# Kernel tuning notes

Hardware: AMD Instinct MI355X
Metric: run time of the kernel (lower is better)

## Reference

```python
import jax, jax.numpy as jnp
import numpy as np

STATE_DIM, FAST, SLOW, ACT, HID = 256, 32, 16, 4, 256
B, T = 256, 512


def _gelu(x):
    return jax.nn.gelu(x, approximate=False)


def _gru_cell(x, h, wih, whh, bih, bhh):
    # torch GRUCell: r,z,n gates; weights are [3H, in]/[3H, H]
    gi = x @ wih.T + bih
    gh = h @ whh.T + bhh
    ir, iz, inn = jnp.split(gi, 3, axis=-1)
    hr, hz, hn = jnp.split(gh, 3, axis=-1)
    r = jax.nn.sigmoid(ir + hr)
    z = jax.nn.sigmoid(iz + hz)
    n = jnp.tanh(inn + r * hn)
    return (1.0 - z) * n + z * h


def setup_inputs() -> dict:
    key = jax.random.key(0)
    ks = jax.random.split(key, 32)
    s = 0.05
    d = {
        'states': jax.random.normal(ks[0], (B, T, STATE_DIM), jnp.float32),
        'actions': jax.random.normal(ks[1], (B, T, ACT), jnp.float32),
        'noise_fast': jax.random.normal(ks[2], (B, T, FAST), jnp.float32),
        'noise_slow': jax.random.normal(ks[3], (B, T, SLOW), jnp.float32),
        # fast encoder: Linear(256,256) GELU Linear(256,64)
        'fe_w1': jax.random.normal(ks[4], (HID, STATE_DIM)) * s,
        'fe_b1': jnp.zeros((HID,)),
        'fe_w2': jax.random.normal(ks[5], (FAST * 2, HID)) * s,
        'fe_b2': jnp.zeros((FAST * 2,)),
        # fast GRUCell(in=36, h=32)
        'fg_wih': jax.random.normal(ks[6], (3 * FAST, FAST + ACT)) * s,
        'fg_whh': jax.random.normal(ks[7], (3 * FAST, FAST)) * s,
        'fg_bih': jnp.zeros((3 * FAST,)),
        'fg_bhh': jnp.zeros((3 * FAST,)),
        # slow encoder: Linear(288,128) GELU Linear(128,32)
        'se_w1': jax.random.normal(ks[8], (HID // 2, STATE_DIM + FAST)) * s,
        'se_b1': jnp.zeros((HID // 2,)),
        'se_w2': jax.random.normal(ks[9], (SLOW * 2, HID // 2)) * s,
        'se_b2': jnp.zeros((SLOW * 2,)),
        # slow GRUCell(in=48, h=16)
        'sg_wih': jax.random.normal(ks[10], (3 * SLOW, SLOW + FAST)) * s,
        'sg_whh': jax.random.normal(ks[11], (3 * SLOW, SLOW)) * s,
        'sg_bih': jnp.zeros((3 * SLOW,)),
        'sg_bhh': jnp.zeros((3 * SLOW,)),
        # decoder: Linear(48,256) GELU Linear(256,256)
        'de_w1': jax.random.normal(ks[12], (HID, FAST + SLOW)) * s,
        'de_b1': jnp.zeros((HID,)),
        'de_w2': jax.random.normal(ks[13], (STATE_DIM, HID)) * s,
        'de_b2': jnp.zeros((STATE_DIM,)),
        'slow_update_rate': jnp.asarray(0.1, jnp.float32),
    }
    return d


def _forward(states, actions, noise_fast, noise_slow,
             fe_w1, fe_b1, fe_w2, fe_b2, fg_wih, fg_whh, fg_bih, fg_bhh,
             se_w1, se_b1, se_w2, se_b2, sg_wih, sg_whh, sg_bih, sg_bhh,
             de_w1, de_b1, de_w2, de_b2, slow_update_rate):
    Bn = states.shape[0]
    upd = jax.nn.sigmoid(slow_update_rate)

    def step(carry, xs):
        z_fast, z_slow = carry
        state, action, nf, ns = xs  # [B, ...] per-timestep slices
        # fast encoder + reparameterization
        fp = _gelu(state @ fe_w1.T + fe_b1) @ fe_w2.T + fe_b2
        f_mean, f_lv = jnp.split(fp, 2, axis=-1)
        z_fast_new = f_mean + jnp.exp(0.5 * f_lv) * nf
        z_fast = _gru_cell(jnp.concatenate([z_fast_new, action], -1), z_fast,
                           fg_wih, fg_whh, fg_bih, fg_bhh)
        # slow encoder + reparameterization
        sp = _gelu(jnp.concatenate([state, z_fast], -1) @ se_w1.T + se_b1) @ se_w2.T + se_b2
        s_mean, s_lv = jnp.split(sp, 2, axis=-1)
        z_slow_new = s_mean + jnp.exp(0.5 * s_lv) * ns
        z_slow_trans = _gru_cell(jnp.concatenate([z_slow_new, z_fast], -1), z_slow,
                                 sg_wih, sg_whh, sg_bih, sg_bhh)
        z_slow = upd * z_slow_trans + (1.0 - upd) * z_slow
        # decoder
        pred = _gelu(jnp.concatenate([z_fast, z_slow], -1) @ de_w1.T + de_b1) @ de_w2.T + de_b2
        return (z_fast, z_slow), (z_fast, z_slow, pred)

    init = (jnp.zeros((Bn, FAST), states.dtype), jnp.zeros((Bn, SLOW), states.dtype))
    xs = (states.swapaxes(0, 1), actions.swapaxes(0, 1),
          noise_fast.swapaxes(0, 1), noise_slow.swapaxes(0, 1))  # time-major [T,B,*]
    _, (zf, zs, preds) = jax.lax.scan(step, init, xs)
    return (preds.swapaxes(0, 1), zf.swapaxes(0, 1), zs.swapaxes(0, 1))


def reference(states, actions, noise_fast, noise_slow,
              fe_w1, fe_b1, fe_w2, fe_b2, fg_wih, fg_whh, fg_bih, fg_bhh,
              se_w1, se_b1, se_w2, se_b2, sg_wih, sg_whh, sg_bih, sg_bhh,
              de_w1, de_b1, de_w2, de_b2, slow_update_rate):
    # returns (predictions [B,T,state_dim], fast_latents [B,T,32], slow_latents [B,T,16])
    return _forward(states, actions, noise_fast, noise_slow,
                    fe_w1, fe_b1, fe_w2, fe_b2, fg_wih, fg_whh, fg_bih, fg_bhh,
                    se_w1, se_b1, se_w2, se_b2, sg_wih, sg_whh, sg_bih, sg_bhh,
                    de_w1, de_b1, de_w2, de_b2, slow_update_rate)
```

## Files before the change

kernel.cpp:

```cpp
#include <hip/hip_runtime.h>

typedef unsigned short u16t;
typedef __attribute__((ext_vector_type(8))) short bf16x8;
typedef __attribute__((ext_vector_type(4))) float f32x4;

#define DI static __device__ __forceinline__

constexpr int Bn = 256, Tn = 512;
constexpr long Rn = (long)Bn * Tn;

DI float b2f(u16t u){ union{unsigned u32; float f;} v; v.u32 = ((unsigned)u)<<16; return v.f; }
DI u16t f2b(float f){ union{float fp; unsigned u;} v; v.fp=f; return (u16t)((v.u + 0x7fffu + ((v.u>>16)&1u))>>16); }
DI float fsigm(float x){ return __builtin_amdgcn_rcpf(1.f + __expf(-x)); }
DI float ftanh(float x){ float e = __expf(2.f*x); return 1.f - 2.f*__builtin_amdgcn_rcpf(e+1.f); }
DI float fgelu(float x){
  float t = 0.7978845608028654f*x*(1.f + 0.044715f*x*x);
  return x*(1.f - __builtin_amdgcn_rcpf(__expf(2.f*t)+1.f));
}
DI f32x4 mfma16(bf16x8 a, bf16x8 b, f32x4 c){ return __builtin_amdgcn_mfma_f32_16x16x32_bf16(a,b,c,0,0,0); }
DI bf16x8 ldw8(const float* p){
  f32x4 a = *(const f32x4*)p, b = *(const f32x4*)(p+4);
  bf16x8 o;
  o[0]=(short)f2b(a[0]); o[1]=(short)f2b(a[1]); o[2]=(short)f2b(a[2]); o[3]=(short)f2b(a[3]);
  o[4]=(short)f2b(b[0]); o[5]=(short)f2b(b[1]); o[6]=(short)f2b(b[2]); o[7]=(short)f2b(b[3]);
  return o;
}
DI bf16x8 zero8(){ bf16x8 v; v[0]=0;v[1]=0;v[2]=0;v[3]=0;v[4]=0;v[5]=0;v[6]=0;v[7]=0; return v; }

__global__ __launch_bounds__(256) void k_pre(
    const float* __restrict__ states, const float* __restrict__ nfast,
    const float* __restrict__ fe_w1, const float* __restrict__ fe_b1,
    const float* __restrict__ fe_w2, const float* __restrict__ fe_b2,
    const float* __restrict__ se_w1, const float* __restrict__ se_b1,
    u16t* __restrict__ ws_zfn, u16t* __restrict__ ws_se1)
{
  __shared__ __align__(16) u16t s_x[64*256];
  __shared__ __align__(16) u16t s_h[64*256];
  const int tid = threadIdx.x;
  const int lane = tid & 63, wave = tid >> 6;
  const int l15 = lane & 15, lh = lane >> 4;
  const long row0 = (long)blockIdx.x * 64;

  #pragma unroll
  for (int i=0;i<8;i++){
    int c = tid + i*256;
    int row = c >> 5, col = (c & 31) << 3;
    bf16x8 v = ldw8(states + (row0+row)*256 + col);
    *(bf16x8*)&s_x[row*256 + (col ^ ((row&7)<<3))] = v;
  }
  __syncthreads();

  const int wrow = wave*16;
  const int arow = wrow + l15;
  f32x4 acc1[16], acc3[8];
  #pragma unroll
  for (int nt=0;nt<16;nt++){ float bv = fe_b1[nt*16+l15]; acc1[nt] = (f32x4){bv,bv,bv,bv}; }
  #pragma unroll
  for (int nt=0;nt<8;nt++){ float bv = se_b1[nt*16+l15]; acc3[nt] = (f32x4){bv,bv,bv,bv}; }
  #pragma unroll
  for (int kt=0;kt<8;kt++){
    int acol = kt*32 + lh*8;
    bf16x8 af = *(const bf16x8*)&s_x[arow*256 + (acol ^ ((arow&7)<<3))];
    #pragma unroll
    for (int nt=0;nt<16;nt++){
      bf16x8 bw = ldw8(fe_w1 + (nt*16+l15)*256 + acol);
      acc1[nt] = mfma16(af, bw, acc1[nt]);
    }
    #pragma unroll
    for (int nt=0;nt<8;nt++){
      bf16x8 bw = ldw8(se_w1 + (nt*16+l15)*288 + acol);
      acc3[nt] = mfma16(af, bw, acc3[nt]);
    }
  }
  #pragma unroll
  for (int nt=0;nt<8;nt++){
    #pragma unroll
    for (int r=0;r<4;r++){
      int row = wrow + lh*4 + r;
      ws_se1[(row0+row)*128 + nt*16+l15] = f2b(acc3[nt][r]);
    }
  }
  #pragma unroll
  for (int nt=0;nt<16;nt++){
    #pragma unroll
    for (int r=0;r<4;r++){
      int row = wrow + lh*4 + r; int col = nt*16 + l15;
      s_h[row*256 + (col ^ ((row&7)<<3))] = f2b(fgelu(acc1[nt][r]));
    }
  }
  __syncthreads();
  f32x4 acc2[4];
  #pragma unroll
  for (int a=0;a<4;a++){ float bv = fe_b2[a*16+l15]; acc2[a] = (f32x4){bv,bv,bv,bv}; }
  #pragma unroll
  for (int kt=0;kt<8;kt++){
    int acol = kt*32 + lh*8;
    bf16x8 af = *(const bf16x8*)&s_h[arow*256 + (acol ^ ((arow&7)<<3))];
    #pragma unroll
    for (int a=0;a<4;a++){
      bf16x8 bw = ldw8(fe_w2 + (a*16+l15)*256 + acol);
      acc2[a] = mfma16(af, bw, acc2[a]);
    }
  }
  #pragma unroll
  for (int a=0;a<2;a++){
    #pragma unroll
    for (int r=0;r<4;r++){
      int row = wrow + lh*4 + r; int col = a*16 + l15;
      float nfv = nfast[(row0+row)*32 + col];
      float zv = acc2[a][r] + __expf(0.5f*acc2[a+2][r])*nfv;
      ws_zfn[(row0+row)*32 + col] = f2b(zv);
    }
  }
}

__global__ __launch_bounds__(64,1) void k_rec(
  const u16t* __restrict__ ws_zfn, const u16t* __restrict__ ws_se1,
  const float* __restrict__ actions, const float* __restrict__ noise_slow,
  const float* __restrict__ fg_wih, const float* __restrict__ fg_whh,
  const float* __restrict__ fg_bih, const float* __restrict__ fg_bhh,
  const float* __restrict__ se_w1, const float* __restrict__ se_w2, const float* __restrict__ se_b2,
  const float* __restrict__ sg_wih, const float* __restrict__ sg_whh,
  const float* __restrict__ sg_bih, const float* __restrict__ sg_bhh,
  const float* __restrict__ updp,
  float* __restrict__ out_zf, float* __restrict__ out_zs)
{
  __shared__ __align__(16) u16t  zfa [16*64];
  __shared__ __align__(16) u16t  hzf [16*64];
  __shared__ __align__(16) u16t  se1b[16*128];
  __shared__ __align__(16) float nsb [16*16];
  __shared__ __align__(16) u16t  hidb[16*128];
  __shared__ __align__(16) u16t  zsb2[16*32];
  const int lane = threadIdx.x;
  const int l15 = lane & 15, lh = lane >> 4;
  const long b0 = (long)blockIdx.x * 16;

  bf16x8 Fwih[6][2], Fwhh[6], Fsw1[8], Fsw2[2][4], Fsgi[3][2], Fsgh[3];
  #pragma unroll
  for (int nt=0;nt<6;nt++){
    Fwih[nt][0] = ldw8(fg_wih + (nt*16+l15)*36 + lh*8);
    bf16x8 v = zero8();
    if (lh==0){
      #pragma unroll
      for (int e=0;e<4;e++) v[e] = (short)f2b(fg_wih[(nt*16+l15)*36 + 32 + e]);
    }
    Fwih[nt][1] = v;
    Fwhh[nt] = ldw8(fg_whh + (nt*16+l15)*32 + lh*8);
  }
  #pragma unroll
  for (int nt=0;nt<8;nt++) Fsw1[nt] = ldw8(se_w1 + (nt*16+l15)*288 + 256 + lh*8);
  #pragma unroll
  for (int nt=0;nt<2;nt++){
    #pragma unroll
    for (int kt=0;kt<4;kt++) Fsw2[nt][kt] = ldw8(se_w2 + (nt*16+l15)*128 + kt*32 + lh*8);
  }
  #pragma unroll
  for (int nt=0;nt<3;nt++){
    #pragma unroll
    for (int kt=0;kt<2;kt++){
      bf16x8 v = zero8();
      if (!(kt==1 && lh>=2)) v = ldw8(sg_wih + (nt*16+l15)*48 + kt*32 + lh*8);
      Fsgi[nt][kt] = v;
    }
    {
      bf16x8 v = zero8();
      if (lh < 2) v = ldw8(sg_whh + (nt*16+l15)*16 + lh*8);
      Fsgh[nt] = v;
    }
  }
  float bih_c[6], bhh_c[6], seb2_c[2], sgbi_c[3], sgbh_c[3];
  #pragma unroll
  for (int nt=0;nt<6;nt++){ bih_c[nt] = fg_bih[nt*16+l15]; bhh_c[nt] = fg_bhh[nt*16+l15]; }
  #pragma unroll
  for (int nt=0;nt<2;nt++) seb2_c[nt] = se_b2[nt*16+l15];
  #pragma unroll
  for (int nt=0;nt<3;nt++){ sgbi_c[nt]=sg_bih[nt*16+l15]; sgbh_c[nt]=sg_bhh[nt*16+l15]; }
  const float upd = fsigm(updp[0]);

  for (int e=0;e<16;e++){ zfa[lane*16+e]=0; hzf[lane*16+e]=0; }
  for (int e=0;e<8;e++) zsb2[lane*8+e]=0;
  float zf_r[2][4] = {{0,0,0,0},{0,0,0,0}};
  float zs_r[4] = {0,0,0,0};

  bf16x8 pf_zfn, pf_se[4]; float pf_act; f32x4 pf_ns;
  const int prow = lane >> 2, pq = lane & 3;
  auto pfload = [&](int tt){
    pf_zfn = *(const bf16x8*)(ws_zfn + ((b0+prow)*Tn + tt)*32 + pq*8);
    #pragma unroll
    for (int i=0;i<4;i++){ int c = i*64+lane; int row = c>>4; int off=(c&15)*8;
      pf_se[i] = *(const bf16x8*)(ws_se1 + ((b0+row)*Tn + tt)*128 + off); }
    pf_act = actions[((b0+prow)*Tn + tt)*4 + pq];
    pf_ns  = *(const f32x4*)(noise_slow + ((b0+prow)*Tn + tt)*16 + pq*4);
  };
  pfload(0);

  for (int t=0; t<Tn; t++){
    *(bf16x8*)&zfa[prow*64 + pq*8] = pf_zfn;
    zfa[prow*64 + 32 + pq] = f2b(pf_act);
    #pragma unroll
    for (int i=0;i<4;i++) *(bf16x8*)&se1b[(i*64+lane)*8] = pf_se[i];
    *(f32x4*)&nsb[prow*16 + pq*4] = pf_ns;
    __syncthreads();
    if (t+1 < Tn) pfload(t+1);

    {
      f32x4 gi[6], gh[6];
      #pragma unroll
      for (int nt=0;nt<6;nt++){ float bi=bih_c[nt], bh=bhh_c[nt];
        gi[nt]=(f32x4){bi,bi,bi,bi}; gh[nt]=(f32x4){bh,bh,bh,bh}; }
      #pragma unroll
      for (int kt=0;kt<2;kt++){
        bf16x8 ax = *(const bf16x8*)&zfa[l15*64 + kt*32 + lh*8];
        #pragma unroll
        for (int nt=0;nt<6;nt++) gi[nt] = mfma16(ax, Fwih[nt][kt], gi[nt]);
      }
      {
        bf16x8 az = *(const bf16x8*)&hzf[l15*64 + 16 + lh*8];
        #pragma unroll
        for (int nt=0;nt<6;nt++) gh[nt] = mfma16(az, Fwhh[nt], gh[nt]);
      }
      #pragma unroll
      for (int a=0;a<2;a++){
        #pragma unroll
        for (int r=0;r<4;r++){
          int row = lh*4+r; int cg = a*16+l15;
          float rg = fsigm(gi[a][r]   + gh[a][r]);
          float zg = fsigm(gi[2+a][r] + gh[2+a][r]);
          float ng = ftanh(gi[4+a][r] + rg*gh[4+a][r]);
          float hv = (1.f-zg)*ng + zg*zf_r[a][r];
          zf_r[a][r] = hv;
          hzf[row*64 + 16 + cg] = f2b(hv);
          out_zf[((b0+row)*Tn + t)*32 + cg] = hv;
        }
      }
    }
    __syncthreads();
    {
      bf16x8 azf2 = *(const bf16x8*)&hzf[l15*64 + 16 + lh*8];
      f32x4 se[8];
      #pragma unroll
      for (int nt=0;nt<8;nt++){
        f32x4 c;
        #pragma unroll
        for (int r=0;r<4;r++) c[r] = b2f(se1b[(lh*4+r)*128 + nt*16+l15]);
        se[nt] = mfma16(azf2, Fsw1[nt], c);
      }
      #pragma unroll
      for (int nt=0;nt<8;nt++){
        #pragma unroll
        for (int r=0;r<4;r++)
          hidb[(lh*4+r)*128 + nt*16+l15] = f2b(fgelu(se[nt][r]));
      }
    }
    __syncthreads();
    {
      f32x4 sp[2];
      #pragma unroll
      for (int nt=0;nt<2;nt++){ float bv=seb2_c[nt]; sp[nt]=(f32x4){bv,bv,bv,bv}; }
      #pragma unroll
      for (int kt=0;kt<4;kt++){
        bf16x8 ah = *(const bf16x8*)&hidb[l15*128 + kt*32 + lh*8];
        #pragma unroll
        for (int nt=0;nt<2;nt++) sp[nt] = mfma16(ah, Fsw2[nt][kt], sp[nt]);
      }
      #pragma unroll
      for (int r=0;r<4;r++){
        int row = lh*4+r;
        float nsv = nsb[row*16 + l15];
        float zn = sp[0][r] + __expf(0.5f*sp[1][r])*nsv;
        hzf[row*64 + l15] = f2b(zn);
      }
    }
    __syncthreads();
    {
      f32x4 gi2[3], gh2[3];
      #pragma unroll
      for (int nt=0;nt<3;nt++){ float bi=sgbi_c[nt], bh=sgbh_c[nt];
        gi2[nt]=(f32x4){bi,bi,bi,bi}; gh2[nt]=(f32x4){bh,bh,bh,bh}; }
      {
        bf16x8 azs = *(const bf16x8*)&zsb2[l15*32 + lh*8];
        #pragma unroll
        for (int nt=0;nt<3;nt++) gh2[nt] = mfma16(azs, Fsgh[nt], gh2[nt]);
      }
      #pragma unroll
      for (int kt=0;kt<2;kt++){
        bf16x8 ax = *(const bf16x8*)&hzf[l15*64 + kt*32 + lh*8];
        #pragma unroll
        for (int nt=0;nt<3;nt++) gi2[nt] = mfma16(ax, Fsgi[nt][kt], gi2[nt]);
      }
      #pragma unroll
      for (int r=0;r<4;r++){
        int row = lh*4+r;
        float rg = fsigm(gi2[0][r] + gh2[0][r]);
        float zg = fsigm(gi2[1][r] + gh2[1][r]);
        float ng = ftanh(gi2[2][r] + rg*gh2[2][r]);
        float zt = (1.f-zg)*ng + zg*zs_r[r];
        float zn = upd*zt + (1.f-upd)*zs_r[r];
        zs_r[r] = zn;
        zsb2[row*32 + l15] = f2b(zn);
        out_zs[((b0+row)*Tn + t)*16 + l15] = zn;
      }
    }
    __syncthreads();
  }
}

__global__ __launch_bounds__(256) void k_dec(
  const float* __restrict__ izf, const float* __restrict__ izs,
  const float* __restrict__ de_w1, const float* __restrict__ de_b1,
  const float* __restrict__ de_w2, const float* __restrict__ de_b2,
  float* __restrict__ preds)
{
  __shared__ __align__(16) u16t s_a[64*64];
  __shared__ __align__(16) u16t s_h[64*256];
  const int tid = threadIdx.x;
  const int lane = tid & 63, wave = tid >> 6;
  const int l15 = lane & 15, lh = lane >> 4;
  const long row0 = (long)blockIdx.x * 64;

  { int row = tid >> 2, col = (tid & 3) << 3;
    bf16x8 v = ldw8(izf + (row0+row)*32 + col);
    *(bf16x8*)&s_a[row*64 + (col ^ ((row&7)<<3))] = v; }
  if (tid < 128){
    int row = tid >> 1, col = 32 + ((tid & 1) << 3);
    bf16x8 v = ldw8(izs + (row0+row)*16 + ((tid&1)<<3));
    *(bf16x8*)&s_a[row*64 + (col ^ ((row&7)<<3))] = v;
  } else {
    int t2 = tid - 128;
    int row = t2 >> 1, col = 48 + ((t2 & 1) << 3);
    bf16x8 v = zero8();
    *(bf16x8*)&s_a[row*64 + (col ^ ((row&7)<<3))] = v;
  }
  __syncthreads();

  const int wrow = wave*16;
  const int arow = wrow + l15;
  f32x4 acc[16];
  #pragma unroll
  for (int nt=0;nt<16;nt++){ float bv = de_b1[nt*16+l15]; acc[nt] = (f32x4){bv,bv,bv,bv}; }
  #pragma unroll
  for (int kt=0;kt<2;kt++){
    int acol = kt*32 + lh*8;
    bf16x8 af = *(const bf16x8*)&s_a[arow*64 + (acol ^ ((arow&7)<<3))];
    #pragma unroll
    for (int nt=0;nt<16;nt++){
      bf16x8 bw = zero8();
      if (!(kt==1 && lh>=2)) bw = ldw8(de_w1 + (nt*16+l15)*48 + acol);
      acc[nt] = mfma16(af, bw, acc[nt]);
    }
  }
  #pragma unroll
  for (int nt=0;nt<16;nt++){
    #pragma unroll
    for (int r=0;r<4;r++){
      int row = wrow + lh*4 + r; int col = nt*16 + l15;
      s_h[row*256 + (col ^ ((row&7)<<3))] = f2b(fgelu(acc[nt][r]));
    }
  }
  __syncthreads();
  f32x4 a2[16];
  #pragma unroll
  for (int nt=0;nt<16;nt++){ float bv = de_b2[nt*16+l15]; a2[nt] = (f32x4){bv,bv,bv,bv}; }
  #pragma unroll
  for (int kt=0;kt<8;kt++){
    int acol = kt*32 + lh*8;
    bf16x8 af = *(const bf16x8*)&s_h[arow*256 + (acol ^ ((arow&7)<<3))];
    #pragma unroll
    for (int nt=0;nt<16;nt++){
      bf16x8 bw = ldw8(de_w2 + (nt*16+l15)*256 + acol);
      a2[nt] = mfma16(af, bw, a2[nt]);
    }
  }
  #pragma unroll
  for (int nt=0;nt<16;nt++){
    #pragma unroll
    for (int r=0;r<4;r++){
      int row = wrow + lh*4 + r;
      preds[(row0+row)*256 + nt*16+l15] = a2[nt][r];
    }
  }
}

extern "C" void kernel_launch(void* const* d_in, const int* in_sizes, int n_in,
                              void* d_out, int out_size, void* d_ws, size_t ws_size,
                              hipStream_t stream)
{
  if (n_in < 25 || in_sizes[0] != (int)(Rn*256) || in_sizes[8] != 96*36 ||
      in_sizes[12] != 128*288 || in_sizes[20] != 256*48 || in_sizes[24] != 1)
    return;
  if (out_size != (int)(Rn*304))
    return;

  const float* states = (const float*)d_in[0];
  const float* actions= (const float*)d_in[1];
  const float* nfast  = (const float*)d_in[2];
  const float* nslow  = (const float*)d_in[3];
  const float* fe_w1  = (const float*)d_in[4];
  const float* fe_b1  = (const float*)d_in[5];
  const float* fe_w2  = (const float*)d_in[6];
  const float* fe_b2  = (const float*)d_in[7];
  const float* fg_wih = (const float*)d_in[8];
  const float* fg_whh = (const float*)d_in[9];
  const float* fg_bih = (const float*)d_in[10];
  const float* fg_bhh = (const float*)d_in[11];
  const float* se_w1  = (const float*)d_in[12];
  const float* se_b1  = (const float*)d_in[13];
  const float* se_w2  = (const float*)d_in[14];
  const float* se_b2  = (const float*)d_in[15];
  const float* sg_wih = (const float*)d_in[16];
  const float* sg_whh = (const float*)d_in[17];
  const float* sg_bih = (const float*)d_in[18];
  const float* sg_bhh = (const float*)d_in[19];
  const float* de_w1  = (const float*)d_in[20];
  const float* de_b1  = (const float*)d_in[21];
  const float* de_w2  = (const float*)d_in[22];
  const float* de_b2  = (const float*)d_in[23];
  const float* updp   = (const float*)d_in[24];

  float* preds = (float*)d_out;
  float* ozf = preds + Rn*256;
  float* ozs = ozf + Rn*32;

  size_t need = (size_t)Rn*320;
  u16t* ws_zfn; u16t* ws_se1;
  if (ws_size >= need){
    ws_zfn = (u16t*)d_ws;
    ws_se1 = ws_zfn + Rn*32;
  } else {
    ws_zfn = (u16t*)preds;
    ws_se1 = ws_zfn + Rn*32;
  }

  k_pre<<<(int)(Rn/64), 256, 0, stream>>>(states, nfast,
      fe_w1, fe_b1, fe_w2, fe_b2, se_w1, se_b1, ws_zfn, ws_se1);
  k_rec<<<Bn/16, 64, 0, stream>>>(ws_zfn, ws_se1, actions, nslow,
      fg_wih, fg_whh, fg_bih, fg_bhh, se_w1, se_w2, se_b2,
      sg_wih, sg_whh, sg_bih, sg_bhh, updp, ozf, ozs);
  k_dec<<<(int)(Rn/64), 256, 0, stream>>>(ozf, ozs, de_w1, de_b1, de_w2, de_b2, preds);
}
```

Before: 2.312 ms.

## Keep recurrent GRU state in registers via transposed MFMA and ds_bpermute shuffles

The recurrent kernel now computes transposed products (weights as the A operand, activations as B), so each lane holds one batch row's outputs. Inter-stage activations are exchanged with ds_bpermute instead of shared memory, which removes all LDS buffers and the four per-step __syncthreads. The precomputed slow-encoder workspace is written in a permuted column order so each lane can load its slice directly, and outputs are stored as float4. The weight conversion also switches to truncating bf16 packing, which slightly changes rounding.

```diff
diff --git a/kernel.cpp b/kernel.cpp
--- a/kernel.cpp
+++ b/kernel.cpp
@@ -18,12 +18,20 @@
   return x*(1.f - __builtin_amdgcn_rcpf(__expf(2.f*t)+1.f));
 }
 DI f32x4 mfma16(bf16x8 a, bf16x8 b, f32x4 c){ return __builtin_amdgcn_mfma_f32_16x16x32_bf16(a,b,c,0,0,0); }
+DI unsigned pk2(float a, float b){
+  union{float f; unsigned u;} x, y; x.f=a; y.f=b;
+  return (x.u>>16) | (y.u & 0xffff0000u);
+}
+DI unsigned pkr(float a, float b){ return (unsigned)f2b(a) | ((unsigned)f2b(b)<<16); }
+DI bf16x8 mk8(unsigned w0,unsigned w1,unsigned w2,unsigned w3){
+  union{unsigned u[4]; bf16x8 v;} z; z.u[0]=w0; z.u[1]=w1; z.u[2]=w2; z.u[3]=w3; return z.v;
+}
+DI unsigned bperm(int srcLane, unsigned v){
+  return (unsigned)__builtin_amdgcn_ds_bpermute(srcLane<<2, (int)v);
+}
 DI bf16x8 ldw8(const float* p){
   f32x4 a = *(const f32x4*)p, b = *(const f32x4*)(p+4);
-  bf16x8 o;
-  o[0]=(short)f2b(a[0]); o[1]=(short)f2b(a[1]); o[2]=(short)f2b(a[2]); o[3]=(short)f2b(a[3]);
-  o[4]=(short)f2b(b[0]); o[5]=(short)f2b(b[1]); o[6]=(short)f2b(b[2]); o[7]=(short)f2b(b[3]);
-  return o;
+  return mk8(pk2(a[0],a[1]), pk2(a[2],a[3]), pk2(b[0],b[1]), pk2(b[2],b[3]));
 }
 DI bf16x8 zero8(){ bf16x8 v; v[0]=0;v[1]=0;v[2]=0;v[3]=0;v[4]=0;v[5]=0;v[6]=0;v[7]=0; return v; }
 
@@ -77,7 +85,7 @@
     #pragma unroll
     for (int r=0;r<4;r++){
       int row = wrow + lh*4 + r;
-      ws_se1[(row0+row)*128 + nt*16+l15] = f2b(acc3[nt][r]);
+      ws_se1[(row0+row)*128 + (l15>>2)*32 + nt*4 + (l15&3)] = f2b(acc3[nt][r]);
     }
   }
   #pragma unroll
@@ -125,183 +133,215 @@
   const float* __restrict__ updp,
   float* __restrict__ out_zf, float* __restrict__ out_zs)
 {
-  __shared__ __align__(16) u16t  zfa [16*64];
-  __shared__ __align__(16) u16t  hzf [16*64];
-  __shared__ __align__(16) u16t  se1b[16*128];
-  __shared__ __align__(16) float nsb [16*16];
-  __shared__ __align__(16) u16t  hidb[16*128];
-  __shared__ __align__(16) u16t  zsb2[16*32];
   const int lane = threadIdx.x;
   const int l15 = lane & 15, lh = lane >> 4;
   const long b0 = (long)blockIdx.x * 16;
-
-  bf16x8 Fwih[6][2], Fwhh[6], Fsw1[8], Fsw2[2][4], Fsgi[3][2], Fsgh[3];
+  const long rowT = (b0 + l15) * (long)Tn;
+
+  bf16x8 Awih[6][2], Awhh[6], Awse[8], Awsp[2][4], Awsg[3][2], Awsh[3];
   #pragma unroll
   for (int nt=0;nt<6;nt++){
-    Fwih[nt][0] = ldw8(fg_wih + (nt*16+l15)*36 + lh*8);
+    Awih[nt][0] = ldw8(fg_wih + (nt*16+l15)*36 + lh*8);
     bf16x8 v = zero8();
     if (lh==0){
       #pragma unroll
       for (int e=0;e<4;e++) v[e] = (short)f2b(fg_wih[(nt*16+l15)*36 + 32 + e]);
     }
-    Fwih[nt][1] = v;
-    Fwhh[nt] = ldw8(fg_whh + (nt*16+l15)*32 + lh*8);
-  }
-  #pragma unroll
-  for (int nt=0;nt<8;nt++) Fsw1[nt] = ldw8(se_w1 + (nt*16+l15)*288 + 256 + lh*8);
+    Awih[nt][1] = v;
+    Awhh[nt] = ldw8(fg_whh + (nt*16+l15)*32 + lh*8);
+  }
+  #pragma unroll
+  for (int nt=0;nt<8;nt++) Awse[nt] = ldw8(se_w1 + (nt*16+l15)*288 + 256 + lh*8);
   #pragma unroll
   for (int nt=0;nt<2;nt++){
     #pragma unroll
-    for (int kt=0;kt<4;kt++) Fsw2[nt][kt] = ldw8(se_w2 + (nt*16+l15)*128 + kt*32 + lh*8);
+    for (int kt=0;kt<4;kt++) Awsp[nt][kt] = ldw8(se_w2 + (nt*16+l15)*128 + kt*32 + lh*8);
   }
   #pragma unroll
   for (int nt=0;nt<3;nt++){
-    #pragma unroll
-    for (int kt=0;kt<2;kt++){
-      bf16x8 v = zero8();
-      if (!(kt==1 && lh>=2)) v = ldw8(sg_wih + (nt*16+l15)*48 + kt*32 + lh*8);
-      Fsgi[nt][kt] = v;
-    }
-    {
-      bf16x8 v = zero8();
-      if (lh < 2) v = ldw8(sg_whh + (nt*16+l15)*16 + lh*8);
-      Fsgh[nt] = v;
-    }
-  }
-  float bih_c[6], bhh_c[6], seb2_c[2], sgbi_c[3], sgbh_c[3];
-  #pragma unroll
-  for (int nt=0;nt<6;nt++){ bih_c[nt] = fg_bih[nt*16+l15]; bhh_c[nt] = fg_bhh[nt*16+l15]; }
-  #pragma unroll
-  for (int nt=0;nt<2;nt++) seb2_c[nt] = se_b2[nt*16+l15];
-  #pragma unroll
-  for (int nt=0;nt<3;nt++){ sgbi_c[nt]=sg_bih[nt*16+l15]; sgbh_c[nt]=sg_bhh[nt*16+l15]; }
+    Awsg[nt][0] = ldw8(sg_wih + (nt*16+l15)*48 + lh*8);
+    bf16x8 v = zero8();
+    if (lh < 2) v = ldw8(sg_wih + (nt*16+l15)*48 + 32 + lh*8);
+    Awsg[nt][1] = v;
+    bf16x8 w = zero8();
+    if (lh < 2) w = ldw8(sg_whh + (nt*16+l15)*16 + lh*8);
+    Awsh[nt] = w;
+  }
+  float bih_l[6][4], bhh_l[6][4], bsp_l[2][4], bsg_l[3][4], bsh_l[3][4];
+  #pragma unroll
+  for (int nt=0;nt<6;nt++){
+    #pragma unroll
+    for (int r=0;r<4;r++){ bih_l[nt][r]=fg_bih[nt*16+lh*4+r]; bhh_l[nt][r]=fg_bhh[nt*16+lh*4+r]; }
+  }
+  #pragma unroll
+  for (int nt=0;nt<2;nt++){
+    #pragma unroll
+    for (int r=0;r<4;r++) bsp_l[nt][r]=se_b2[nt*16+lh*4+r];
+  }
+  #pragma unroll
+  for (int nt=0;nt<3;nt++){
+    #pragma unroll
+    for (int r=0;r<4;r++){ bsg_l[nt][r]=sg_bih[nt*16+lh*4+r]; bsh_l[nt][r]=sg_bhh[nt*16+lh*4+r]; }
+  }
   const float upd = fsigm(updp[0]);
 
-  for (int e=0;e<16;e++){ zfa[lane*16+e]=0; hzf[lane*16+e]=0; }
-  for (int e=0;e<8;e++) zsb2[lane*8+e]=0;
+  unsigned zfw[4] = {0,0,0,0};
+  unsigned zsw[4] = {0,0,0,0};
   float zf_r[2][4] = {{0,0,0,0},{0,0,0,0}};
   float zs_r[4] = {0,0,0,0};
 
-  bf16x8 pf_zfn, pf_se[4]; float pf_act; f32x4 pf_ns;
-  const int prow = lane >> 2, pq = lane & 3;
+  bf16x8 pf_zfn, pf_se[4]; f32x4 pf_act, pf_ns;
   auto pfload = [&](int tt){
-    pf_zfn = *(const bf16x8*)(ws_zfn + ((b0+prow)*Tn + tt)*32 + pq*8);
-    #pragma unroll
-    for (int i=0;i<4;i++){ int c = i*64+lane; int row = c>>4; int off=(c&15)*8;
-      pf_se[i] = *(const bf16x8*)(ws_se1 + ((b0+row)*Tn + tt)*128 + off); }
-    pf_act = actions[((b0+prow)*Tn + tt)*4 + pq];
-    pf_ns  = *(const f32x4*)(noise_slow + ((b0+prow)*Tn + tt)*16 + pq*4);
+    pf_zfn = *(const bf16x8*)(ws_zfn + (rowT+tt)*32 + lh*8);
+    #pragma unroll
+    for (int i=0;i<4;i++) pf_se[i] = *(const bf16x8*)(ws_se1 + (rowT+tt)*128 + lh*32 + i*8);
+    pf_act = *(const f32x4*)(actions + (rowT+tt)*4);
+    pf_ns  = *(const f32x4*)(noise_slow + (rowT+tt)*16 + lh*4);
   };
   pfload(0);
 
   for (int t=0; t<Tn; t++){
-    *(bf16x8*)&zfa[prow*64 + pq*8] = pf_zfn;
-    zfa[prow*64 + 32 + pq] = f2b(pf_act);
-    #pragma unroll
-    for (int i=0;i<4;i++) *(bf16x8*)&se1b[(i*64+lane)*8] = pf_se[i];
-    *(f32x4*)&nsb[prow*16 + pq*4] = pf_ns;
-    __syncthreads();
+    bf16x8 zfnB = pf_zfn;
+    bf16x8 seP0 = pf_se[0], seP1 = pf_se[1], seP2 = pf_se[2], seP3 = pf_se[3];
+    f32x4 actv = pf_act, nsv = pf_ns;
     if (t+1 < Tn) pfload(t+1);
 
+    bf16x8 actB = zero8();
+    if (lh==0) actB = mk8(pk2(actv[0],actv[1]), pk2(actv[2],actv[3]), 0, 0);
+
+    f32x4 gi[6], gh[6];
+    #pragma unroll
+    for (int nt=0;nt<6;nt++){
+      gi[nt] = (f32x4){bih_l[nt][0],bih_l[nt][1],bih_l[nt][2],bih_l[nt][3]};
+      gh[nt] = (f32x4){bhh_l[nt][0],bhh_l[nt][1],bhh_l[nt][2],bhh_l[nt][3]};
+    }
+    bf16x8 zfB = mk8(zfw[0],zfw[1],zfw[2],zfw[3]);
+    #pragma unroll
+    for (int nt=0;nt<6;nt++) gi[nt] = mfma16(Awih[nt][0], zfnB, gi[nt]);
+    #pragma unroll
+    for (int nt=0;nt<6;nt++) gi[nt] = mfma16(Awih[nt][1], actB, gi[nt]);
+    #pragma unroll
+    for (int nt=0;nt<6;nt++) gh[nt] = mfma16(Awhh[nt], zfB, gh[nt]);
+    float hv[2][4];
+    #pragma unroll
+    for (int a=0;a<2;a++){
+      #pragma unroll
+      for (int r=0;r<4;r++){
+        float rg = fsigm(gi[a][r]   + gh[a][r]);
+        float zg = fsigm(gi[2+a][r] + gh[2+a][r]);
+        float ng = ftanh(gi[4+a][r] + rg*gh[4+a][r]);
+        float h2 = (1.f-zg)*ng + zg*zf_r[a][r];
+        zf_r[a][r] = h2; hv[a][r] = h2;
+      }
+      f32x4 o = (f32x4){hv[a][0],hv[a][1],hv[a][2],hv[a][3]};
+      *(f32x4*)(out_zf + (rowT+t)*32 + a*16 + lh*4) = o;
+    }
     {
-      f32x4 gi[6], gh[6];
-      #pragma unroll
-      for (int nt=0;nt<6;nt++){ float bi=bih_c[nt], bh=bhh_c[nt];
-        gi[nt]=(f32x4){bi,bi,bi,bi}; gh[nt]=(f32x4){bh,bh,bh,bh}; }
-      #pragma unroll
-      for (int kt=0;kt<2;kt++){
-        bf16x8 ax = *(const bf16x8*)&zfa[l15*64 + kt*32 + lh*8];
-        #pragma unroll
-        for (int nt=0;nt<6;nt++) gi[nt] = mfma16(ax, Fwih[nt][kt], gi[nt]);
-      }
-      {
-        bf16x8 az = *(const bf16x8*)&hzf[l15*64 + 16 + lh*8];
-        #pragma unroll
-        for (int nt=0;nt<6;nt++) gh[nt] = mfma16(az, Fwhh[nt], gh[nt]);
-      }
-      #pragma unroll
-      for (int a=0;a<2;a++){
-        #pragma unroll
-        for (int r=0;r<4;r++){
-          int row = lh*4+r; int cg = a*16+l15;
-          float rg = fsigm(gi[a][r]   + gh[a][r]);
-          float zg = fsigm(gi[2+a][r] + gh[2+a][r]);
-          float ng = ftanh(gi[4+a][r] + rg*gh[4+a][r]);
-          float hv = (1.f-zg)*ng + zg*zf_r[a][r];
-          zf_r[a][r] = hv;
-          hzf[row*64 + 16 + cg] = f2b(hv);
-          out_zf[((b0+row)*Tn + t)*32 + cg] = hv;
-        }
-      }
-    }
-    __syncthreads();
+      unsigned P00=pkr(hv[0][0],hv[0][1]), P01=pkr(hv[0][2],hv[0][3]);
+      unsigned P10=pkr(hv[1][0],hv[1][1]), P11=pkr(hv[1][2],hv[1][3]);
+      #pragma unroll
+      for (int w=0;w<4;w++){
+        int srcl = ((2*(lh&1) + (w>>1))<<4) + l15;
+        unsigned r0 = bperm(srcl, (w&1)?P01:P00);
+        unsigned r1 = bperm(srcl, (w&1)?P11:P10);
+        zfw[w] = (lh>>1) ? r1 : r0;
+      }
+    }
+    bf16x8 zfBn = mk8(zfw[0],zfw[1],zfw[2],zfw[3]);
+
+    unsigned HP[8][2];
+    #pragma unroll
+    for (int nt=0;nt<8;nt++){
+      f32x4 c;
+      #pragma unroll
+      for (int r=0;r<4;r++){
+        int e = (nt&1)*4 + r;
+        u16t sv = (nt>>1)==0 ? (u16t)seP0[e] : (nt>>1)==1 ? (u16t)seP1[e]
+                 : (nt>>1)==2 ? (u16t)seP2[e] : (u16t)seP3[e];
+        c[r] = b2f(sv);
+      }
+      f32x4 se = mfma16(Awse[nt], zfBn, c);
+      float g0=fgelu(se[0]), g1=fgelu(se[1]), g2=fgelu(se[2]), g3=fgelu(se[3]);
+      HP[nt][0]=pk2(g0,g1); HP[nt][1]=pk2(g2,g3);
+    }
+    bf16x8 hidB[4];
+    #pragma unroll
+    for (int kt=0;kt<4;kt++){
+      unsigned ww[4];
+      #pragma unroll
+      for (int w=0;w<4;w++){
+        int srcl = ((2*(lh&1) + (w>>1))<<4) + l15;
+        unsigned r0 = bperm(srcl, HP[2*kt  ][w&1]);
+        unsigned r1 = bperm(srcl, HP[2*kt+1][w&1]);
+        ww[w] = (lh>>1) ? r1 : r0;
+      }
+      hidB[kt] = mk8(ww[0],ww[1],ww[2],ww[3]);
+    }
+
+    f32x4 sp[2];
+    #pragma unroll
+    for (int nt=0;nt<2;nt++) sp[nt] = (f32x4){bsp_l[nt][0],bsp_l[nt][1],bsp_l[nt][2],bsp_l[nt][3]};
+    #pragma unroll
+    for (int kt=0;kt<4;kt++){
+      #pragma unroll
+      for (int nt=0;nt<2;nt++) sp[nt] = mfma16(Awsp[nt][kt], hidB[kt], sp[nt]);
+    }
+    float zsn[4];
+    #pragma unroll
+    for (int r=0;r<4;r++) zsn[r] = sp[0][r] + __expf(0.5f*sp[1][r])*nsv[r];
+    bf16x8 sgB0, sgB1;
     {
-      bf16x8 azf2 = *(const bf16x8*)&hzf[l15*64 + 16 + lh*8];
-      f32x4 se[8];
-      #pragma unroll
-      for (int nt=0;nt<8;nt++){
-        f32x4 c;
-        #pragma unroll
-        for (int r=0;r<4;r++) c[r] = b2f(se1b[(lh*4+r)*128 + nt*16+l15]);
-        se[nt] = mfma16(azf2, Fsw1[nt], c);
-      }
-      #pragma unroll
-      for (int nt=0;nt<8;nt++){
-        #pragma unroll
-        for (int r=0;r<4;r++)
-          hidb[(lh*4+r)*128 + nt*16+l15] = f2b(fgelu(se[nt][r]));
-      }
-    }
-    __syncthreads();
+      unsigned QZ0=pk2(zsn[0],zsn[1]), QZ1=pk2(zsn[2],zsn[3]);
+      unsigned w0_[4], w1_[4];
+      int srcF = ((lh^2)<<4) + l15;
+      #pragma unroll
+      for (int w=0;w<4;w++){
+        int srcZ = ((2*(lh&1) + (w>>1))<<4) + l15;
+        unsigned vz = bperm(srcZ, (w&1)?QZ1:QZ0);
+        unsigned vf = bperm(srcF, zfw[w]);
+        w0_[w] = (lh<2) ? vz : vf;
+        w1_[w] = (lh<2) ? vf : 0u;
+      }
+      sgB0 = mk8(w0_[0],w0_[1],w0_[2],w0_[3]);
+      sgB1 = mk8(w1_[0],w1_[1],w1_[2],w1_[3]);
+    }
+
+    f32x4 gi2[3], gh2[3];
+    #pragma unroll
+    for (int nt=0;nt<3;nt++){
+      gi2[nt] = (f32x4){bsg_l[nt][0],bsg_l[nt][1],bsg_l[nt][2],bsg_l[nt][3]};
+      gh2[nt] = (f32x4){bsh_l[nt][0],bsh_l[nt][1],bsh_l[nt][2],bsh_l[nt][3]};
+    }
+    bf16x8 zsB = mk8(zsw[0],zsw[1],zsw[2],zsw[3]);
+    #pragma unroll
+    for (int nt=0;nt<3;nt++) gh2[nt] = mfma16(Awsh[nt], zsB, gh2[nt]);
+    #pragma unroll
+    for (int nt=0;nt<3;nt++) gi2[nt] = mfma16(Awsg[nt][0], sgB0, gi2[nt]);
+    #pragma unroll
+    for (int nt=0;nt<3;nt++) gi2[nt] = mfma16(Awsg[nt][1], sgB1, gi2[nt]);
+    float zn[4];
+    #pragma unroll
+    for (int r=0;r<4;r++){
+      float rg = fsigm(gi2[0][r] + gh2[0][r]);
+      float zg = fsigm(gi2[1][r] + gh2[1][r]);
+      float ng = ftanh(gi2[2][r] + rg*gh2[2][r]);
+      float zt = (1.f-zg)*ng + zg*zs_r[r];
+      float z2 = upd*zt + (1.f-upd)*zs_r[r];
+      zs_r[r] = z2; zn[r] = z2;
+    }
     {
-      f32x4 sp[2];
-      #pragma unroll
-      for (int nt=0;nt<2;nt++){ float bv=seb2_c[nt]; sp[nt]=(f32x4){bv,bv,bv,bv}; }
-      #pragma unroll
-      for (int kt=0;kt<4;kt++){
-        bf16x8 ah = *(const bf16x8*)&hidb[l15*128 + kt*32 + lh*8];
-        #pragma unroll
-        for (int nt=0;nt<2;nt++) sp[nt] = mfma16(ah, Fsw2[nt][kt], sp[nt]);
-      }
-      #pragma unroll
-      for (int r=0;r<4;r++){
-        int row = lh*4+r;
-        float nsv = nsb[row*16 + l15];
-        float zn = sp[0][r] + __expf(0.5f*sp[1][r])*nsv;
-        hzf[row*64 + l15] = f2b(zn);
-      }
-    }
-    __syncthreads();
+      f32x4 o = (f32x4){zn[0],zn[1],zn[2],zn[3]};
+      *(f32x4*)(out_zs + (rowT+t)*16 + lh*4) = o;
+    }
     {
-      f32x4 gi2[3], gh2[3];
-      #pragma unroll
-      for (int nt=0;nt<3;nt++){ float bi=sgbi_c[nt], bh=sgbh_c[nt];
-        gi2[nt]=(f32x4){bi,bi,bi,bi}; gh2[nt]=(f32x4){bh,bh,bh,bh}; }
-      {
-        bf16x8 azs = *(const bf16x8*)&zsb2[l15*32 + lh*8];
-        #pragma unroll
-        for (int nt=0;nt<3;nt++) gh2[nt] = mfma16(azs, Fsgh[nt], gh2[nt]);
-      }
-      #pragma unroll
-      for (int kt=0;kt<2;kt++){
-        bf16x8 ax = *(const bf16x8*)&hzf[l15*64 + kt*32 + lh*8];
-        #pragma unroll
-        for (int nt=0;nt<3;nt++) gi2[nt] = mfma16(ax, Fsgi[nt][kt], gi2[nt]);
-      }
-      #pragma unroll
-      for (int r=0;r<4;r++){
-        int row = lh*4+r;
-        float rg = fsigm(gi2[0][r] + gh2[0][r]);
-        float zg = fsigm(gi2[1][r] + gh2[1][r]);
-        float ng = ftanh(gi2[2][r] + rg*gh2[2][r]);
-        float zt = (1.f-zg)*ng + zg*zs_r[r];
-        float zn = upd*zt + (1.f-upd)*zs_r[r];
-        zs_r[r] = zn;
-        zsb2[row*32 + l15] = f2b(zn);
-        out_zs[((b0+row)*Tn + t)*16 + l15] = zn;
-      }
-    }
-    __syncthreads();
+      unsigned QS0=pkr(zn[0],zn[1]), QS1=pkr(zn[2],zn[3]);
+      #pragma unroll
+      for (int w=0;w<4;w++){
+        int srcl = ((2*(lh&1) + (w>>1))<<4) + l15;
+        unsigned v = bperm(srcl, (w&1)?QS1:QS0);
+        zsw[w] = (lh<2) ? v : 0u;
+      }
+    }
   }
 }
 
```

Result: faster. 2.003 ms (-13.4%).

## Run recurrence with one batch row per wave using scalar FMA dot products

Applied to the files above, without the earlier changes.

The recurrent kernel is restructured so each 64-lane block handles a single batch element instead of 16. Gate and encoder matmuls become per-lane FMA dot products against bf16-packed weights held in registers, replacing MFMA tiles. Workgroup barriers are replaced by an LDS waitcnt plus scheduling barrier, which is valid because the block is a single wave. The grid grows from 16 to 256 blocks to fill more CUs, at the cost of more per-lane serial FMAs on the critical path and higher register pressure.

```diff
diff --git a/kernel.cpp b/kernel.cpp
--- a/kernel.cpp
+++ b/kernel.cpp
@@ -3,6 +3,7 @@
 typedef unsigned short u16t;
 typedef __attribute__((ext_vector_type(8))) short bf16x8;
 typedef __attribute__((ext_vector_type(4))) float f32x4;
+typedef __attribute__((ext_vector_type(2))) float f32x2;
 
 #define DI static __device__ __forceinline__
 
@@ -18,14 +19,18 @@
   return x*(1.f - __builtin_amdgcn_rcpf(__expf(2.f*t)+1.f));
 }
 DI f32x4 mfma16(bf16x8 a, bf16x8 b, f32x4 c){ return __builtin_amdgcn_mfma_f32_16x16x32_bf16(a,b,c,0,0,0); }
+DI unsigned pkr(float a, float b){ return (unsigned)f2b(a) | ((unsigned)f2b(b)<<16); }
+DI float plo(unsigned u){ union{unsigned x; float f;} v; v.x = u<<16; return v.f; }
+DI float phi(unsigned u){ union{unsigned x; float f;} v; v.x = u & 0xffff0000u; return v.f; }
+DI bf16x8 mk8(unsigned w0,unsigned w1,unsigned w2,unsigned w3){
+  union{unsigned u[4]; bf16x8 v;} z; z.u[0]=w0; z.u[1]=w1; z.u[2]=w2; z.u[3]=w3; return z.v;
+}
 DI bf16x8 ldw8(const float* p){
   f32x4 a = *(const f32x4*)p, b = *(const f32x4*)(p+4);
-  bf16x8 o;
-  o[0]=(short)f2b(a[0]); o[1]=(short)f2b(a[1]); o[2]=(short)f2b(a[2]); o[3]=(short)f2b(a[3]);
-  o[4]=(short)f2b(b[0]); o[5]=(short)f2b(b[1]); o[6]=(short)f2b(b[2]); o[7]=(short)f2b(b[3]);
-  return o;
+  return mk8(pkr(a[0],a[1]), pkr(a[2],a[3]), pkr(b[0],b[1]), pkr(b[2],b[3]));
 }
 DI bf16x8 zero8(){ bf16x8 v; v[0]=0;v[1]=0;v[2]=0;v[3]=0;v[4]=0;v[5]=0;v[6]=0;v[7]=0; return v; }
+DI void lfence(){ asm volatile("s_waitcnt lgkmcnt(0)" ::: "memory"); __builtin_amdgcn_sched_barrier(0); }
 
 __global__ __launch_bounds__(256) void k_pre(
     const float* __restrict__ states, const float* __restrict__ nfast,
@@ -125,183 +130,154 @@
   const float* __restrict__ updp,
   float* __restrict__ out_zf, float* __restrict__ out_zs)
 {
-  __shared__ __align__(16) u16t  zfa [16*64];
-  __shared__ __align__(16) u16t  hzf [16*64];
-  __shared__ __align__(16) u16t  se1b[16*128];
-  __shared__ __align__(16) float nsb [16*16];
-  __shared__ __align__(16) u16t  hidb[16*128];
-  __shared__ __align__(16) u16t  zsb2[16*32];
+  __shared__ __align__(16) float zfv[32], zsv[16], zfnv[32], actv[4], nsv[16];
+  __shared__ __align__(16) float se1v[128], hidv[128], zsnv[16], spb[32];
+  __shared__ __align__(16) float gsum[64], gni[32], gnh[32], sgib[48], sghb[48];
   const int lane = threadIdx.x;
-  const int l15 = lane & 15, lh = lane >> 4;
-  const long b0 = (long)blockIdx.x * 16;
-
-  bf16x8 Fwih[6][2], Fwhh[6], Fsw1[8], Fsw2[2][4], Fsgi[3][2], Fsgh[3];
-  #pragma unroll
-  for (int nt=0;nt<6;nt++){
-    Fwih[nt][0] = ldw8(fg_wih + (nt*16+l15)*36 + lh*8);
-    bf16x8 v = zero8();
-    if (lh==0){
-      #pragma unroll
-      for (int e=0;e<4;e++) v[e] = (short)f2b(fg_wih[(nt*16+l15)*36 + 32 + e]);
-    }
-    Fwih[nt][1] = v;
-    Fwhh[nt] = ldw8(fg_whh + (nt*16+l15)*32 + lh*8);
-  }
-  #pragma unroll
-  for (int nt=0;nt<8;nt++) Fsw1[nt] = ldw8(se_w1 + (nt*16+l15)*288 + 256 + lh*8);
-  #pragma unroll
-  for (int nt=0;nt<2;nt++){
-    #pragma unroll
-    for (int kt=0;kt<4;kt++) Fsw2[nt][kt] = ldw8(se_w2 + (nt*16+l15)*128 + kt*32 + lh*8);
-  }
-  #pragma unroll
-  for (int nt=0;nt<3;nt++){
-    #pragma unroll
-    for (int kt=0;kt<2;kt++){
-      bf16x8 v = zero8();
-      if (!(kt==1 && lh>=2)) v = ldw8(sg_wih + (nt*16+l15)*48 + kt*32 + lh*8);
-      Fsgi[nt][kt] = v;
-    }
+  const int l31 = lane & 31, hf = lane >> 5;
+  const long base = (long)blockIdx.x * Tn;
+
+  unsigned wihP[18], whhP[16], wihH[9], whhH[8], wseP[2][16], wspP[32], wsgiP[24], wsghP[8];
+  #pragma unroll
+  for (int p=0;p<18;p++) wihP[p] = pkr(fg_wih[lane*36+2*p], fg_wih[lane*36+2*p+1]);
+  #pragma unroll
+  for (int p=0;p<16;p++) whhP[p] = pkr(fg_whh[lane*32+2*p], fg_whh[lane*32+2*p+1]);
+  #pragma unroll
+  for (int p=0;p<9;p++){ int k = hf*18+2*p;
+    wihH[p] = pkr(fg_wih[(64+l31)*36 + k], fg_wih[(64+l31)*36 + k+1]); }
+  #pragma unroll
+  for (int p=0;p<8;p++){ int k = hf*16+2*p;
+    whhH[p] = pkr(fg_whh[(64+l31)*32 + k], fg_whh[(64+l31)*32 + k+1]); }
+  #pragma unroll
+  for (int jj=0;jj<2;jj++){
+    #pragma unroll
+    for (int p=0;p<16;p++)
+      wseP[jj][p] = pkr(se_w1[(lane+jj*64)*288 + 256 + 2*p], se_w1[(lane+jj*64)*288 + 256 + 2*p+1]);
+  }
+  #pragma unroll
+  for (int p=0;p<32;p++)
+    wspP[p] = pkr(se_w2[l31*128 + hf*64 + 2*p], se_w2[l31*128 + hf*64 + 2*p+1]);
+  if (lane < 48){
+    #pragma unroll
+    for (int p=0;p<24;p++) wsgiP[p] = pkr(sg_wih[lane*48+2*p], sg_wih[lane*48+2*p+1]);
+    #pragma unroll
+    for (int p=0;p<8;p++)  wsghP[p] = pkr(sg_whh[lane*16+2*p], sg_whh[lane*16+2*p+1]);
+  }
+  const float bsum  = fg_bih[lane] + fg_bhh[lane];
+  const float bni2  = fg_bih[64+l31], bnh2 = fg_bhh[64+l31];
+  const float seb2L = se_b2[l31];
+  const float sgbiL = sg_bih[lane<48?lane:47], sgbhL = sg_bhh[lane<48?lane:47];
+  const float upd = fsigm(updp[0]);
+
+  if (lane < 32) zfv[lane] = 0.f;
+  if (lane < 16) zsv[lane] = 0.f;
+
+  u16t pzfn = 0, ps0 = 0, ps1 = 0; float pact = 0.f, pns = 0.f;
+  auto pf = [&](int tt){
+    if (lane < 32) pzfn = ws_zfn[(base+tt)*32 + lane];
+    ps0 = ws_se1[(base+tt)*128 + lane];
+    ps1 = ws_se1[(base+tt)*128 + 64 + lane];
+    if (lane < 4)  pact = actions[(base+tt)*4 + lane];
+    if (lane < 16) pns  = noise_slow[(base+tt)*16 + lane];
+  };
+  pf(0);
+
+  for (int t=0; t<Tn; t++){
+    if (lane < 32) zfnv[lane] = b2f(pzfn);
+    se1v[lane] = b2f(ps0); se1v[64+lane] = b2f(ps1);
+    if (lane < 4)  actv[lane] = pact;
+    if (lane < 16) nsv[lane] = pns;
+    lfence();
+    if (t+1 < Tn) pf(t+1);
+
     {
-      bf16x8 v = zero8();
-      if (lh < 2) v = ldw8(sg_whh + (nt*16+l15)*16 + lh*8);
-      Fsgh[nt] = v;
-    }
-  }
-  float bih_c[6], bhh_c[6], seb2_c[2], sgbi_c[3], sgbh_c[3];
-  #pragma unroll
-  for (int nt=0;nt<6;nt++){ bih_c[nt] = fg_bih[nt*16+l15]; bhh_c[nt] = fg_bhh[nt*16+l15]; }
-  #pragma unroll
-  for (int nt=0;nt<2;nt++) seb2_c[nt] = se_b2[nt*16+l15];
-  #pragma unroll
-  for (int nt=0;nt<3;nt++){ sgbi_c[nt]=sg_bih[nt*16+l15]; sgbh_c[nt]=sg_bhh[nt*16+l15]; }
-  const float upd = fsigm(updp[0]);
-
-  for (int e=0;e<16;e++){ zfa[lane*16+e]=0; hzf[lane*16+e]=0; }
-  for (int e=0;e<8;e++) zsb2[lane*8+e]=0;
-  float zf_r[2][4] = {{0,0,0,0},{0,0,0,0}};
-  float zs_r[4] = {0,0,0,0};
-
-  bf16x8 pf_zfn, pf_se[4]; float pf_act; f32x4 pf_ns;
-  const int prow = lane >> 2, pq = lane & 3;
-  auto pfload = [&](int tt){
-    pf_zfn = *(const bf16x8*)(ws_zfn + ((b0+prow)*Tn + tt)*32 + pq*8);
-    #pragma unroll
-    for (int i=0;i<4;i++){ int c = i*64+lane; int row = c>>4; int off=(c&15)*8;
-      pf_se[i] = *(const bf16x8*)(ws_se1 + ((b0+row)*Tn + tt)*128 + off); }
-    pf_act = actions[((b0+prow)*Tn + tt)*4 + pq];
-    pf_ns  = *(const f32x4*)(noise_slow + ((b0+prow)*Tn + tt)*16 + pq*4);
-  };
-  pfload(0);
-
-  for (int t=0; t<Tn; t++){
-    *(bf16x8*)&zfa[prow*64 + pq*8] = pf_zfn;
-    zfa[prow*64 + 32 + pq] = f2b(pf_act);
-    #pragma unroll
-    for (int i=0;i<4;i++) *(bf16x8*)&se1b[(i*64+lane)*8] = pf_se[i];
-    *(f32x4*)&nsb[prow*16 + pq*4] = pf_ns;
-    __syncthreads();
-    if (t+1 < Tn) pfload(t+1);
-
+      float s = bsum;
+      #pragma unroll
+      for (int p=0;p<18;p++){
+        f32x2 x = (p<16) ? *(const f32x2*)&zfnv[2*p] : *(const f32x2*)&actv[2*(p-16)];
+        s += plo(wihP[p])*x[0] + phi(wihP[p])*x[1];
+      }
+      #pragma unroll
+      for (int p=0;p<16;p++){
+        f32x2 x = *(const f32x2*)&zfv[2*p];
+        s += plo(whhP[p])*x[0] + phi(whhP[p])*x[1];
+      }
+      gsum[lane] = s;
+      float si = 0.f, sh = 0.f;
+      #pragma unroll
+      for (int p=0;p<9;p++){
+        int k = hf*18 + 2*p;
+        f32x2 x = (k < 32) ? *(const f32x2*)&zfnv[k] : *(const f32x2*)&actv[k-32];
+        si += plo(wihH[p])*x[0] + phi(wihH[p])*x[1];
+      }
+      #pragma unroll
+      for (int p=0;p<8;p++){
+        f32x2 x = *(const f32x2*)&zfv[hf*16 + 2*p];
+        sh += plo(whhH[p])*x[0] + phi(whhH[p])*x[1];
+      }
+      si += __shfl_xor(si, 32);
+      sh += __shfl_xor(sh, 32);
+      if (lane < 32){ gni[lane] = si + bni2; gnh[lane] = sh + bnh2; }
+    }
+    lfence();
+    if (lane < 32){
+      float r = fsigm(gsum[lane]);
+      float z = fsigm(gsum[32+lane]);
+      float n = ftanh(gni[lane] + r*gnh[lane]);
+      float h2 = (1.f-z)*n + z*zfv[lane];
+      zfv[lane] = h2;
+      out_zf[(base+t)*32 + lane] = h2;
+    }
+    lfence();
+    #pragma unroll
+    for (int jj=0;jj<2;jj++){
+      float s = se1v[lane + jj*64];
+      #pragma unroll
+      for (int p=0;p<16;p++){
+        f32x2 x = *(const f32x2*)&zfv[2*p];
+        s += plo(wseP[jj][p])*x[0] + phi(wseP[jj][p])*x[1];
+      }
+      hidv[lane + jj*64] = fgelu(s);
+    }
+    lfence();
     {
-      f32x4 gi[6], gh[6];
-      #pragma unroll
-      for (int nt=0;nt<6;nt++){ float bi=bih_c[nt], bh=bhh_c[nt];
-        gi[nt]=(f32x4){bi,bi,bi,bi}; gh[nt]=(f32x4){bh,bh,bh,bh}; }
-      #pragma unroll
-      for (int kt=0;kt<2;kt++){
-        bf16x8 ax = *(const bf16x8*)&zfa[l15*64 + kt*32 + lh*8];
-        #pragma unroll
-        for (int nt=0;nt<6;nt++) gi[nt] = mfma16(ax, Fwih[nt][kt], gi[nt]);
-      }
-      {
-        bf16x8 az = *(const bf16x8*)&hzf[l15*64 + 16 + lh*8];
-        #pragma unroll
-        for (int nt=0;nt<6;nt++) gh[nt] = mfma16(az, Fwhh[nt], gh[nt]);
-      }
-      #pragma unroll
-      for (int a=0;a<2;a++){
-        #pragma unroll
-        for (int r=0;r<4;r++){
-          int row = lh*4+r; int cg = a*16+l15;
-          float rg = fsigm(gi[a][r]   + gh[a][r]);
-          float zg = fsigm(gi[2+a][r] + gh[2+a][r]);
-          float ng = ftanh(gi[4+a][r] + rg*gh[4+a][r]);
-          float hv = (1.f-zg)*ng + zg*zf_r[a][r];
-          zf_r[a][r] = hv;
-          hzf[row*64 + 16 + cg] = f2b(hv);
-          out_zf[((b0+row)*Tn + t)*32 + cg] = hv;
-        }
-      }
-    }
-    __syncthreads();
-    {
-      bf16x8 azf2 = *(const bf16x8*)&hzf[l15*64 + 16 + lh*8];
-      f32x4 se[8];
-      #pragma unroll
-      for (int nt=0;nt<8;nt++){
-        f32x4 c;
-        #pragma unroll
-        for (int r=0;r<4;r++) c[r] = b2f(se1b[(lh*4+r)*128 + nt*16+l15]);
-        se[nt] = mfma16(azf2, Fsw1[nt], c);
-      }
-      #pragma unroll
-      for (int nt=0;nt<8;nt++){
-        #pragma unroll
-        for (int r=0;r<4;r++)
-          hidb[(lh*4+r)*128 + nt*16+l15] = f2b(fgelu(se[nt][r]));
-      }
-    }
-    __syncthreads();
-    {
-      f32x4 sp[2];
-      #pragma unroll
-      for (int nt=0;nt<2;nt++){ float bv=seb2_c[nt]; sp[nt]=(f32x4){bv,bv,bv,bv}; }
-      #pragma unroll
-      for (int kt=0;kt<4;kt++){
-        bf16x8 ah = *(const bf16x8*)&hidb[l15*128 + kt*32 + lh*8];
-        #pragma unroll
-        for (int nt=0;nt<2;nt++) sp[nt] = mfma16(ah, Fsw2[nt][kt], sp[nt]);
-      }
-      #pragma unroll
-      for (int r=0;r<4;r++){
-        int row = lh*4+r;
-        float nsv = nsb[row*16 + l15];
-        float zn = sp[0][r] + __expf(0.5f*sp[1][r])*nsv;
-        hzf[row*64 + l15] = f2b(zn);
-      }
-    }
-    __syncthreads();
-    {
-      f32x4 gi2[3], gh2[3];
-      #pragma unroll
-      for (int nt=0;nt<3;nt++){ float bi=sgbi_c[nt], bh=sgbh_c[nt];
-        gi2[nt]=(f32x4){bi,bi,bi,bi}; gh2[nt]=(f32x4){bh,bh,bh,bh}; }
-      {
-        bf16x8 azs = *(const bf16x8*)&zsb2[l15*32 + lh*8];
-        #pragma unroll
-        for (int nt=0;nt<3;nt++) gh2[nt] = mfma16(azs, Fsgh[nt], gh2[nt]);
-      }
-      #pragma unroll
-      for (int kt=0;kt<2;kt++){
-        bf16x8 ax = *(const bf16x8*)&hzf[l15*64 + kt*32 + lh*8];
-        #pragma unroll
-        for (int nt=0;nt<3;nt++) gi2[nt] = mfma16(ax, Fsgi[nt][kt], gi2[nt]);
-      }
-      #pragma unroll
-      for (int r=0;r<4;r++){
-        int row = lh*4+r;
-        float rg = fsigm(gi2[0][r] + gh2[0][r]);
-        float zg = fsigm(gi2[1][r] + gh2[1][r]);
-        float ng = ftanh(gi2[2][r] + rg*gh2[2][r]);
-        float zt = (1.f-zg)*ng + zg*zs_r[r];
-        float zn = upd*zt + (1.f-upd)*zs_r[r];
-        zs_r[r] = zn;
-        zsb2[row*32 + l15] = f2b(zn);
-        out_zs[((b0+row)*Tn + t)*16 + l15] = zn;
-      }
-    }
-    __syncthreads();
+      float s = 0.f;
+      #pragma unroll
+      for (int p=0;p<32;p++){
+        f32x2 x = *(const f32x2*)&hidv[hf*64 + 2*p];
+        s += plo(wspP[p])*x[0] + phi(wspP[p])*x[1];
+      }
+      s += __shfl_xor(s, 32);
+      if (lane < 32) spb[lane] = s + seb2L;
+    }
+    lfence();
+    if (lane < 16) zsnv[lane] = spb[lane] + __expf(0.5f*spb[16+lane])*nsv[lane];
+    lfence();
+    if (lane < 48){
+      float gi = sgbiL, gh = sgbhL;
+      #pragma unroll
+      for (int p=0;p<24;p++){
+        f32x2 x = (p<8) ? *(const f32x2*)&zsnv[2*p] : *(const f32x2*)&zfv[2*p-16];
+        gi += plo(wsgiP[p])*x[0] + phi(wsgiP[p])*x[1];
+      }
+      #pragma unroll
+      for (int p=0;p<8;p++){
+        f32x2 x = *(const f32x2*)&zsv[2*p];
+        gh += plo(wsghP[p])*x[0] + phi(wsghP[p])*x[1];
+      }
+      sgib[lane] = gi; sghb[lane] = gh;
+    }
+    lfence();
+    if (lane < 16){
+      float r = fsigm(sgib[lane] + sghb[lane]);
+      float z = fsigm(sgib[16+lane] + sghb[16+lane]);
+      float n = ftanh(sgib[32+lane] + r*sghb[32+lane]);
+      float zt = (1.f-z)*n + z*zsv[lane];
+      float zn = upd*zt + (1.f-upd)*zsv[lane];
+      zsv[lane] = zn;
+      out_zs[(base+t)*16 + lane] = zn;
+    }
+    lfence();
   }
 }
 
@@ -433,7 +409,7 @@
 
   k_pre<<<(int)(Rn/64), 256, 0, stream>>>(states, nfast,
       fe_w1, fe_b1, fe_w2, fe_b2, se_w1, se_b1, ws_zfn, ws_se1);
-  k_rec<<<Bn/16, 64, 0, stream>>>(ws_zfn, ws_se1, actions, nslow,
+  k_rec<<<Bn, 64, 0, stream>>>(ws_zfn, ws_se1, actions, nslow,
       fg_wih, fg_whh, fg_bih, fg_bhh, se_w1, se_w2, se_b2,
       sg_wih, sg_whh, sg_bih, sg_bhh, updp, ozf, ozs);
   k_dec<<<(int)(Rn/64), 256, 0, stream>>>(ozf, ozs, de_w1, de_b1, de_w2, de_b2, preds);
```

Measured after the change: 2.134 ms. -7.7%, faster.
